# Optimization experiments

Hardware: AMD Instinct MI355X
Metric: run time of the kernel (lower is better)

Reference implementation:

```python
import jax, jax.numpy as jnp
import numpy as np

N = 50000          # nodes
E = 800000         # edges (avg degree 16)
D = 128            # feature dim
MSG_EPS = 1e-7     # GENConv eps added to relu(msg)
SM_EPS = 1e-16     # pyg softmax denominator eps
BN_EPS = 1e-5
LN_EPS = 1e-5


def setup_inputs() -> dict:
    key = jax.random.key(0)
    ks = jax.random.split(key, 6)
    x = jax.random.normal(ks[0], (N, D), dtype=jnp.float32)
    edge_index = jax.random.randint(ks[1], (2, E), 0, N, dtype=jnp.int32)
    t = jnp.array(1.0, dtype=jnp.float32)
    W1 = jax.random.normal(ks[2], (D, 2 * D), dtype=jnp.float32) / np.sqrt(D).astype(np.float32)
    b1 = jnp.zeros((2 * D,), jnp.float32)
    bn_gamma = jnp.ones((2 * D,), jnp.float32)
    bn_beta = jnp.zeros((2 * D,), jnp.float32)
    W2 = jax.random.normal(ks[3], (2 * D, D), dtype=jnp.float32) / np.sqrt(2 * D).astype(np.float32)
    b2 = jnp.zeros((D,), jnp.float32)
    ln_gamma = jnp.ones((D,), jnp.float32)
    ln_beta = jnp.zeros((D,), jnp.float32)
    return {"x": x, "edge_index": edge_index, "t": t, "W1": W1, "b1": b1,
            "bn_gamma": bn_gamma, "bn_beta": bn_beta, "W2": W2, "b2": b2,
            "ln_gamma": ln_gamma, "ln_beta": ln_beta}


def reference(x, edge_index, t, W1, b1, bn_gamma, bn_beta, W2, b2, ln_gamma, ln_beta):
    src, dst = edge_index[0], edge_index[1]
    # --- GENConv message: relu(x_j) + eps  -> [E, D]
    msg = jax.nn.relu(x[src]) + MSG_EPS
    # --- softmax aggregation over incoming edges per dst node, per feature
    logits = t * msg                                            # [E, D]
    seg_max = jax.ops.segment_max(logits, dst, num_segments=N)  # [N, D]
    seg_max = jnp.where(jnp.isfinite(seg_max), seg_max, 0.0)    # empty segments -> 0
    ex = jnp.exp(logits - seg_max[dst])                         # [E, D]
    denom = jax.ops.segment_sum(ex, dst, num_segments=N)        # [N, D]
    alpha = ex / (denom[dst] + SM_EPS)                          # [E, D]
    agg = jax.ops.segment_sum(alpha * msg, dst, num_segments=N) # [N, D]
    # --- GENConv update: MLP(agg + x), MLP = Lin(D,2D)->BN->ReLU->Lin(2D,D)
    h = agg + x
    h = h @ W1 + b1                                             # [N, 2D]
    mu = jnp.mean(h, axis=0)
    var = jnp.var(h, axis=0)
    h = (h - mu) * jax.lax.rsqrt(var + BN_EPS) * bn_gamma + bn_beta
    h = jax.nn.relu(h)
    h = h @ W2 + b2                                             # [N, D]
    # --- LayerNorm -> ReLU -> (dropout p=0 noop) -> residual
    mu2 = jnp.mean(h, axis=-1, keepdims=True)
    var2 = jnp.mean(jnp.square(h - mu2), axis=-1, keepdims=True)
    h = (h - mu2) * jax.lax.rsqrt(var2 + LN_EPS) * ln_gamma + ln_beta
    h = jax.nn.relu(h)
    return x + h
```

## Files before the change

### kernel.cpp

```cpp
#include <hip/hip_runtime.h>

#define D 128
#define D2 256
#define BSH 5
#define BNODES 32
#define NBMAX 2048
#define CAP 640
#define PCHUNK 4096

typedef __attribute__((ext_vector_type(8))) short short8;
typedef __attribute__((ext_vector_type(4))) float f32x4;

__device__ inline unsigned short f2b(float f) {
  unsigned u = __float_as_uint(f);
  unsigned r = (u + 0x7FFFu + ((u >> 16) & 1u)) >> 16;
  return (unsigned short)r;
}
__device__ inline float b2f(unsigned short h) {
  return __uint_as_float(((unsigned)h) << 16);
}
__device__ inline float lo2f(unsigned u) { return __uint_as_float(u << 16); }
__device__ inline float hi2f(unsigned u) { return __uint_as_float(u & 0xffff0000u); }

__global__ void convert_w_kernel(const float* __restrict__ W1,
                                 const float* __restrict__ W2,
                                 unsigned short* __restrict__ W1f,
                                 unsigned short* __restrict__ W2f) {
  int idx = blockIdx.x * 256 + threadIdx.x;
  if (idx < 32768) {
    int k = idx >> 8, n = idx & 255;
    int t = n >> 4, m16 = n & 15;
    int kk = k >> 5, quad = (k >> 3) & 3, j = k & 7;
    W1f[(((t * 4 + kk) * 64 + quad * 16 + m16) << 3) + j] = f2b(W1[idx]);
  } else {
    int i = idx - 32768;
    int k = i >> 7, n = i & 127;
    int t = n >> 4, m16 = n & 15;
    int kk = k >> 5, quad = (k >> 3) & 3, j = k & 7;
    W2f[(((t * 8 + kk) * 64 + quad * 16 + m16) << 3) + j] = f2b(W2[i]);
  }
}

__global__ void mb_kernel(const float* __restrict__ x, unsigned short* __restrict__ mb,
                          int total4) {
  int i = blockIdx.x * 256 + threadIdx.x;
  if (i < total4) {
    float4 v = reinterpret_cast<const float4*>(x)[i];
    unsigned lo = (unsigned)f2b(fmaxf(v.x, 0.f) + 1e-7f) |
                  ((unsigned)f2b(fmaxf(v.y, 0.f) + 1e-7f) << 16);
    unsigned hi = (unsigned)f2b(fmaxf(v.z, 0.f) + 1e-7f) |
                  ((unsigned)f2b(fmaxf(v.w, 0.f) + 1e-7f) << 16);
    reinterpret_cast<uint2*>(mb)[i] = make_uint2(lo, hi);
  } else if (i < total4 + 32) {
    reinterpret_cast<uint2*>(mb)[i] = make_uint2(0u, 0u);
  }
}

__global__ __launch_bounds__(256) void part_kernel(const int* __restrict__ ei,
                                                   int* __restrict__ cursor,
                                                   unsigned* __restrict__ pairbuf,
                                                   int E, int nb) {
  __shared__ int cnt[NBMAX];
  __shared__ int base[NBMAX];
  int tid = threadIdx.x;
  int c0 = blockIdx.x * PCHUNK;
  int nE = min(PCHUNK, E - c0);
  for (int i = tid; i < nb; i += 256) cnt[i] = 0;
  __syncthreads();
  for (int j = tid; j < nE; j += 256) {
    int dst = ei[E + c0 + j];
    atomicAdd(&cnt[dst >> BSH], 1);
  }
  __syncthreads();
  for (int i = tid; i < nb; i += 256) {
    int c = cnt[i];
    base[i] = (c > 0) ? atomicAdd(&cursor[i], c) : 0;
    cnt[i] = 0;
  }
  __syncthreads();
  for (int j = tid; j < nE; j += 256) {
    int e = c0 + j;
    int dst = ei[E + e];
    int src = ei[e];
    int b = dst >> BSH;
    int r = base[b] + atomicAdd(&cnt[b], 1);
    if (r < CAP)
      pairbuf[(size_t)b * CAP + r] =
          (unsigned)src | ((unsigned)(dst & (BNODES - 1)) << 16);
  }
}

__global__ __launch_bounds__(512) void agg2_kernel(const float* __restrict__ x,
                                                   const unsigned short* __restrict__ mb,
                                                   const unsigned* __restrict__ pairbuf,
                                                   const int* __restrict__ cursor,
                                                   const float* __restrict__ tptr,
                                                   unsigned short* __restrict__ h0b, int N) {
  __shared__ int soff[CAP + 4 * BNODES];
  __shared__ int cnt[BNODES], off[BNODES], run[BNODES], pcnt[BNODES];
  int b = blockIdx.x;
  int tid = threadIdx.x;
  int Eb = min(cursor[b], CAP);
  if (tid < BNODES) { cnt[tid] = 0; run[tid] = 0; }
  __syncthreads();
  for (int j = tid; j < Eb; j += 512)
    atomicAdd(&cnt[pairbuf[(size_t)b * CAP + j] >> 16], 1);
  __syncthreads();
  if (tid < BNODES) {
    int c = cnt[tid];
    int pc = (c + 3) & ~3;
    pcnt[tid] = pc;
    int s = pc;
#pragma unroll
    for (int st = 1; st < 32; st <<= 1) {
      int u = __shfl_up(s, st, 32);
      if ((tid & 31) >= st) s += u;
    }
    off[tid] = s - pc;
  }
  __syncthreads();
  for (int j = tid; j < Eb; j += 512) {
    unsigned p = pairbuf[(size_t)b * CAP + j];
    int dl = p >> 16;
    int r = atomicAdd(&run[dl], 1);
    soff[off[dl] + r] = (int)(p & 0xffffu) << 8;
  }
  if (tid < BNODES) {
    int o = off[tid];
    for (int r = cnt[tid]; r < pcnt[tid]; ++r) soff[o + r] = N << 8;
  }
  __syncthreads();

  int w = tid >> 6;
  int l = tid & 63;
  float t = tptr[0];
  int laneoff = l << 2;
  const char* mbase = (const char*)mb;
  for (int ln = w; ln < BNODES; ln += 8) {
    int n = (b << BSH) + ln;
    if (n >= N) continue;
    int s0 = off[ln];
    int dn = pcnt[ln];
    float den0 = 0.f, num0 = 0.f, den1 = 0.f, num1 = 0.f;
    if (dn > 0) {
      unsigned uu[4];
#pragma unroll
      for (int q = 0; q < 4; ++q)
        uu[q] = *(const unsigned*)(mbase + (soff[s0 + q] | laneoff));
      for (int j = 4; j < dn; j += 4) {
        unsigned vv[4];
#pragma unroll
        for (int q = 0; q < 4; ++q)
          vv[q] = *(const unsigned*)(mbase + (soff[s0 + j + q] | laneoff));
#pragma unroll
        for (int q = 0; q < 4; ++q) {
          float m0 = lo2f(uu[q]);
          float m1 = hi2f(uu[q]);
          float e0 = __expf(t * m0);
          float e1 = __expf(t * m1);
          den0 += e0; num0 += e0 * m0;
          den1 += e1; num1 += e1 * m1;
        }
#pragma unroll
        for (int q = 0; q < 4; ++q) uu[q] = vv[q];
      }
#pragma unroll
      for (int q = 0; q < 4; ++q) {
        float m0 = lo2f(uu[q]);
        float m1 = hi2f(uu[q]);
        float e0 = __expf(t * m0);
        float e1 = __expf(t * m1);
        den0 += e0; num0 += e0 * m0;
        den1 += e1; num1 += e1 * m1;
      }
      float fnpad = (float)(dn - cnt[ln]);
      den0 -= fnpad;
      den1 -= fnpad;
    }
    size_t idx = ((size_t)n << 7) + 2 * l;
    float2 xv = *reinterpret_cast<const float2*>(x + idx);
    float v0 = num0 / (den0 + 1e-16f) + xv.x;
    float v1 = num1 / (den1 + 1e-16f) + xv.y;
    *reinterpret_cast<unsigned*>(h0b + idx) =
        (unsigned)f2b(v0) | ((unsigned)f2b(v1) << 16);
  }
}

__global__ __launch_bounds__(256) void gemm1_mfma(
    const unsigned short* __restrict__ h0b, const unsigned short* __restrict__ W1f,
    unsigned short* __restrict__ h1b,
    float* __restrict__ bnsum, float* __restrict__ bnsumsq, int M) {
  __shared__ unsigned short lt[4][64][72];
  int tid = threadIdx.x;
  int w = tid >> 6;
  int l = tid & 63;
  int m16 = l & 15;
  int quad = l >> 4;
  int r0 = blockIdx.x * 64;

  f32x4 acc[4][4];
#pragma unroll
  for (int rt = 0; rt < 4; ++rt)
#pragma unroll
    for (int ct = 0; ct < 4; ++ct) acc[rt][ct] = (f32x4){0.f, 0.f, 0.f, 0.f};

#pragma unroll
  for (int kk = 0; kk < 4; ++kk) {
    short8 bfr[4];
#pragma unroll
    for (int ct = 0; ct < 4; ++ct)
      bfr[ct] = *reinterpret_cast<const short8*>(
          W1f + ((((w * 4 + ct) * 4 + kk) * 64 + l) << 3));
    short8 a[4];
#pragma unroll
    for (int rt = 0; rt < 4; ++rt) {
      int row = min(r0 + rt * 16 + m16, M - 1);
      a[rt] = *reinterpret_cast<const short8*>(h0b + (size_t)row * D + kk * 32 + quad * 8);
    }
#pragma unroll
    for (int rt = 0; rt < 4; ++rt)
#pragma unroll
      for (int ct = 0; ct < 4; ++ct)
        acc[rt][ct] = __builtin_amdgcn_mfma_f32_16x16x32_bf16(a[rt], bfr[ct], acc[rt][ct], 0, 0, 0);
  }

#pragma unroll
  for (int ct = 0; ct < 4; ++ct) {
    int col = w * 64 + ct * 16 + m16;
    float cs = 0.f, cq = 0.f;
#pragma unroll
    for (int rt = 0; rt < 4; ++rt) {
      int rloc = rt * 16 + quad * 4;
#pragma unroll
      for (int reg = 0; reg < 4; ++reg) {
        float val = acc[rt][ct][reg];
        if (r0 + rloc + reg < M) {
          cs += val;
          cq += val * val;
        }
        lt[w][rloc + reg][ct * 16 + m16] = f2b(val);
      }
    }
    cs += __shfl_xor(cs, 16, 64);
    cs += __shfl_xor(cs, 32, 64);
    cq += __shfl_xor(cq, 16, 64);
    cq += __shfl_xor(cq, 32, 64);
    if (quad == 0) {
      atomicAdd(&bnsum[col], cs);
      atomicAdd(&bnsumsq[col], cq);
    }
  }

  int row = r0 + l;
  if (row < M) {
    const unsigned short* src = &lt[w][l][0];
    unsigned short* dst = h1b + (size_t)row * D2 + w * 64;
#pragma unroll
    for (int j = 0; j < 8; ++j)
      *reinterpret_cast<short8*>(dst + j * 8) =
          *reinterpret_cast<const short8*>(src + j * 8);
  }
}

__global__ void bnfinal_kernel(const float* __restrict__ bnsum,
                               const float* __restrict__ bnsumsq,
                               const float* __restrict__ gamma,
                               const float* __restrict__ beta,
                               float* __restrict__ scale,
                               float* __restrict__ shift, int M) {
  int c = threadIdx.x;
  float invM = 1.f / (float)M;
  float mu = bnsum[c] * invM;
  float var = bnsumsq[c] * invM - mu * mu;
  float sc = gamma[c] * rsqrtf(var + 1e-5f);
  scale[c] = sc;
  shift[c] = beta[c] - mu * sc;
}

__global__ __launch_bounds__(256) void bnapply_kernel(
    unsigned short* __restrict__ h1b, const float* __restrict__ scale,
    const float* __restrict__ shift, int total8) {
  int i = blockIdx.x * 256 + threadIdx.x;
  if (i >= total8) return;
  int c0 = (i << 3) & 255;
  f32x4 sc0 = *reinterpret_cast<const f32x4*>(scale + c0);
  f32x4 sc1 = *reinterpret_cast<const f32x4*>(scale + c0 + 4);
  f32x4 sh0 = *reinterpret_cast<const f32x4*>(shift + c0);
  f32x4 sh1 = *reinterpret_cast<const f32x4*>(shift + c0 + 4);
  uint4 raw = reinterpret_cast<const uint4*>(h1b)[i];
  unsigned words[4] = {raw.x, raw.y, raw.z, raw.w};
  uint4 o;
  unsigned ow[4];
#pragma unroll
  for (int p = 0; p < 2; ++p) {
    f32x4 sc = p ? sc1 : sc0;
    f32x4 sh = p ? sh1 : sh0;
#pragma unroll
    for (int q = 0; q < 2; ++q) {
      unsigned u = words[p * 2 + q];
      float v0 = fmaxf(lo2f(u) * sc[q * 2] + sh[q * 2], 0.f);
      float v1 = fmaxf(hi2f(u) * sc[q * 2 + 1] + sh[q * 2 + 1], 0.f);
      ow[p * 2 + q] = (unsigned)f2b(v0) | ((unsigned)f2b(v1) << 16);
    }
  }
  o.x = ow[0]; o.y = ow[1]; o.z = ow[2]; o.w = ow[3];
  reinterpret_cast<uint4*>(h1b)[i] = o;
}

__global__ __launch_bounds__(256) void gemm2_mfma(
    const unsigned short* __restrict__ h1c, const unsigned short* __restrict__ W2f,
    const float* __restrict__ b2, const float* __restrict__ lng,
    const float* __restrict__ lnb, const float* __restrict__ x,
    float* __restrict__ out, int M) {
  __shared__ float lnp[64][2], lnp2[64][2];
  int tid = threadIdx.x;
  int w = tid >> 6;
  int l = tid & 63;
  int m16 = l & 15;
  int quad = l >> 4;
  int rb = w >> 1, cb = w & 1;
  int r00 = blockIdx.x * 64;

  f32x4 acc[2][4];
#pragma unroll
  for (int rt = 0; rt < 2; ++rt)
#pragma unroll
    for (int ct = 0; ct < 4; ++ct) acc[rt][ct] = (f32x4){0.f, 0.f, 0.f, 0.f};

#pragma unroll
  for (int kk = 0; kk < 8; ++kk) {
    short8 a[2];
#pragma unroll
    for (int rt = 0; rt < 2; ++rt) {
      int row = min(r00 + rb * 32 + rt * 16 + m16, M - 1);
      a[rt] = *reinterpret_cast<const short8*>(h1c + (size_t)row * D2 + kk * 32 + quad * 8);
    }
    short8 bfr[4];
#pragma unroll
    for (int ct = 0; ct < 4; ++ct)
      bfr[ct] = *reinterpret_cast<const short8*>(
          W2f + ((((cb * 4 + ct) * 8 + kk) * 64 + l) << 3));
#pragma unroll
    for (int rt = 0; rt < 2; ++rt)
#pragma unroll
      for (int ct = 0; ct < 4; ++ct)
        acc[rt][ct] = __builtin_amdgcn_mfma_f32_16x16x32_bf16(a[rt], bfr[ct], acc[rt][ct], 0, 0, 0);
  }

  float b2v[4], lgv[4], lbv[4];
#pragma unroll
  for (int ct = 0; ct < 4; ++ct) {
    int col = cb * 64 + ct * 16 + m16;
    b2v[ct] = b2[col];
    lgv[ct] = lng[col];
    lbv[ct] = lnb[col];
  }

#pragma unroll
  for (int rt = 0; rt < 2; ++rt) {
#pragma unroll
    for (int reg = 0; reg < 4; ++reg) {
      float s = 0.f, s2 = 0.f;
#pragma unroll
      for (int ct = 0; ct < 4; ++ct) {
        float v = acc[rt][ct][reg] + b2v[ct];
        s += v;
        s2 += v * v;
      }
#pragma unroll
      for (int msk = 1; msk < 16; msk <<= 1) {
        s += __shfl_xor(s, msk, 64);
        s2 += __shfl_xor(s2, msk, 64);
      }
      if (m16 == 0) {
        int rl = rb * 32 + rt * 16 + quad * 4 + reg;
        lnp[rl][cb] = s;
        lnp2[rl][cb] = s2;
      }
    }
  }
  __syncthreads();

#pragma unroll
  for (int rt = 0; rt < 2; ++rt) {
#pragma unroll
    for (int reg = 0; reg < 4; ++reg) {
      int rl = rb * 32 + rt * 16 + quad * 4 + reg;
      int row = r00 + rl;
      float s = lnp[rl][0] + lnp[rl][1];
      float s2 = lnp2[rl][0] + lnp2[rl][1];
      float mu = s * (1.f / 128.f);
      float var = s2 * (1.f / 128.f) - mu * mu;
      float inv = rsqrtf(var + 1e-5f);
      if (row < M) {
#pragma unroll
        for (int ct = 0; ct < 4; ++ct) {
          int col = cb * 64 + ct * 16 + m16;
          float v = acc[rt][ct][reg] + b2v[ct];
          float h = fmaxf((v - mu) * inv * lgv[ct] + lbv[ct], 0.f);
          out[(size_t)row * D + col] = x[(size_t)row * D + col] + h;
        }
      }
    }
  }
}

extern "C" void kernel_launch(void* const* d_in, const int* in_sizes, int n_in,
                              void* d_out, int out_size, void* d_ws, size_t ws_size,
                              hipStream_t stream) {
  const float* x   = (const float*)d_in[0];
  const int*   ei  = (const int*)d_in[1];
  const float* t   = (const float*)d_in[2];
  const float* W1  = (const float*)d_in[3];
  const float* bng = (const float*)d_in[5];
  const float* bnb = (const float*)d_in[6];
  const float* W2  = (const float*)d_in[7];
  const float* b2  = (const float*)d_in[8];
  const float* lng = (const float*)d_in[9];
  const float* lnb = (const float*)d_in[10];
  float* out = (float*)d_out;

  int N = in_sizes[0] / D;
  int E = in_sizes[1] / 2;
  size_t nd = (size_t)N * D;
  int nb = (N + BNODES - 1) >> BSH;

  unsigned short* mb  = (unsigned short*)d_ws;
  unsigned short* h0b = mb + nd + 128;
  unsigned short* h1b = h0b + nd;
  unsigned short* W1f = h1b + 2 * nd;
  unsigned short* W2f = W1f + 32768;
  float* bnsum   = (float*)(W2f + 32768);
  float* bnsumsq = bnsum + D2;
  float* bnscale = bnsumsq + D2;
  float* bnshift = bnscale + D2;
  int* cursor = (int*)(bnshift + D2);
  unsigned* pairbuf = (unsigned*)(cursor + NBMAX);

  hipMemsetAsync(bnsum, 0, (4 * D2 + NBMAX) * sizeof(int), stream);

  convert_w_kernel<<<256, 256, 0, stream>>>(W1, W2, W1f, W2f);
  int total4 = (int)(nd / 4);
  mb_kernel<<<(total4 + 32 + 255) / 256, 256, 0, stream>>>(x, mb, total4);

  part_kernel<<<(E + PCHUNK - 1) / PCHUNK, 256, 0, stream>>>(ei, cursor, pairbuf, E, nb);
  agg2_kernel<<<nb, 512, 0, stream>>>(x, mb, pairbuf, cursor, t, h0b, N);

  gemm1_mfma<<<(N + 63) / 64, 256, 0, stream>>>(h0b, W1f, h1b, bnsum, bnsumsq, N);
  bnfinal_kernel<<<1, 256, 0, stream>>>(bnsum, bnsumsq, bng, bnb, bnscale, bnshift, N);
  int total8 = (int)(2 * nd / 8);
  bnapply_kernel<<<(total8 + 255) / 256, 256, 0, stream>>>(h1b, bnscale, bnshift, total8);
  gemm2_mfma<<<(N + 63) / 64, 256, 0, stream>>>(h1b, W2f, b2, lng, lnb, x, out, N);
}
```

Before: 226.3 us.

## Fuse BN apply into gemm2 and spread BN-stat and cursor atomics

Removes the separate bnapply pass over the 2D-wide hidden buffer. BatchNorm scale/shift plus ReLU are now applied on the fly while loading the A operand in gemm2, with scale and shift staged in shared memory. BN sum and sum-of-squares atomics are spread across 32 replicas keyed by block index and reduced in bnfinal. Partition cursors are strided by 16 ints so they do not share cache lines. This saves one full read/write pass of h1 and a launch, and cuts atomic contention, at the cost of extra ALU work in gemm2's load path and a larger memset.

Result: faster. 211.3 us (-6.7%).

```diff
diff --git a/kernel.cpp b/kernel.cpp
--- a/kernel.cpp
+++ b/kernel.cpp
@@ -7,6 +7,8 @@
 #define NBMAX 2048
 #define CAP 640
 #define PCHUNK 4096
+#define REP 32
+#define CSTRIDE 16
 
 typedef __attribute__((ext_vector_type(8))) short short8;
 typedef __attribute__((ext_vector_type(4))) float f32x4;
@@ -74,7 +76,7 @@
   __syncthreads();
   for (int i = tid; i < nb; i += 256) {
     int c = cnt[i];
-    base[i] = (c > 0) ? atomicAdd(&cursor[i], c) : 0;
+    base[i] = (c > 0) ? atomicAdd(&cursor[i * CSTRIDE], c) : 0;
     cnt[i] = 0;
   }
   __syncthreads();
@@ -100,7 +102,7 @@
   __shared__ int cnt[BNODES], off[BNODES], run[BNODES], pcnt[BNODES];
   int b = blockIdx.x;
   int tid = threadIdx.x;
-  int Eb = min(cursor[b], CAP);
+  int Eb = min(cursor[b * CSTRIDE], CAP);
   if (tid < BNODES) { cnt[tid] = 0; run[tid] = 0; }
   __syncthreads();
   for (int j = tid; j < Eb; j += 512)
@@ -224,6 +226,7 @@
         acc[rt][ct] = __builtin_amdgcn_mfma_f32_16x16x32_bf16(a[rt], bfr[ct], acc[rt][ct], 0, 0, 0);
   }
 
+  int rep = (blockIdx.x & (REP - 1)) << 8;
 #pragma unroll
   for (int ct = 0; ct < 4; ++ct) {
     int col = w * 64 + ct * 16 + m16;
@@ -246,8 +249,8 @@
     cq += __shfl_xor(cq, 16, 64);
     cq += __shfl_xor(cq, 32, 64);
     if (quad == 0) {
-      atomicAdd(&bnsum[col], cs);
-      atomicAdd(&bnsumsq[col], cq);
+      atomicAdd(&bnsum[rep + col], cs);
+      atomicAdd(&bnsumsq[rep + col], cq);
     }
   }
 
@@ -269,51 +272,33 @@
                                float* __restrict__ scale,
                                float* __restrict__ shift, int M) {
   int c = threadIdx.x;
+  float s = 0.f, q = 0.f;
+#pragma unroll
+  for (int r = 0; r < REP; ++r) {
+    s += bnsum[(r << 8) + c];
+    q += bnsumsq[(r << 8) + c];
+  }
   float invM = 1.f / (float)M;
-  float mu = bnsum[c] * invM;
-  float var = bnsumsq[c] * invM - mu * mu;
+  float mu = s * invM;
+  float var = q * invM - mu * mu;
   float sc = gamma[c] * rsqrtf(var + 1e-5f);
   scale[c] = sc;
   shift[c] = beta[c] - mu * sc;
 }
 
-__global__ __launch_bounds__(256) void bnapply_kernel(
-    unsigned short* __restrict__ h1b, const float* __restrict__ scale,
-    const float* __restrict__ shift, int total8) {
-  int i = blockIdx.x * 256 + threadIdx.x;
-  if (i >= total8) return;
-  int c0 = (i << 3) & 255;
-  f32x4 sc0 = *reinterpret_cast<const f32x4*>(scale + c0);
-  f32x4 sc1 = *reinterpret_cast<const f32x4*>(scale + c0 + 4);
-  f32x4 sh0 = *reinterpret_cast<const f32x4*>(shift + c0);
-  f32x4 sh1 = *reinterpret_cast<const f32x4*>(shift + c0 + 4);
-  uint4 raw = reinterpret_cast<const uint4*>(h1b)[i];
-  unsigned words[4] = {raw.x, raw.y, raw.z, raw.w};
-  uint4 o;
-  unsigned ow[4];
-#pragma unroll
-  for (int p = 0; p < 2; ++p) {
-    f32x4 sc = p ? sc1 : sc0;
-    f32x4 sh = p ? sh1 : sh0;
-#pragma unroll
-    for (int q = 0; q < 2; ++q) {
-      unsigned u = words[p * 2 + q];
-      float v0 = fmaxf(lo2f(u) * sc[q * 2] + sh[q * 2], 0.f);
-      float v1 = fmaxf(hi2f(u) * sc[q * 2 + 1] + sh[q * 2 + 1], 0.f);
-      ow[p * 2 + q] = (unsigned)f2b(v0) | ((unsigned)f2b(v1) << 16);
-    }
-  }
-  o.x = ow[0]; o.y = ow[1]; o.z = ow[2]; o.w = ow[3];
-  reinterpret_cast<uint4*>(h1b)[i] = o;
-}
-
 __global__ __launch_bounds__(256) void gemm2_mfma(
-    const unsigned short* __restrict__ h1c, const unsigned short* __restrict__ W2f,
-    const float* __restrict__ b2, const float* __restrict__ lng,
+    const unsigned short* __restrict__ h1b, const unsigned short* __restrict__ W2f,
+    const float* __restrict__ b2, const float* __restrict__ bnscale,
+    const float* __restrict__ bnshift, const float* __restrict__ lng,
     const float* __restrict__ lnb, const float* __restrict__ x,
     float* __restrict__ out, int M) {
   __shared__ float lnp[64][2], lnp2[64][2];
+  __shared__ float sS[D2], sH[D2];
   int tid = threadIdx.x;
+  sS[tid] = bnscale[tid];
+  sH[tid] = bnshift[tid];
+  __syncthreads();
+
   int w = tid >> 6;
   int l = tid & 63;
   int m16 = l & 15;
@@ -329,11 +314,29 @@
 
 #pragma unroll
   for (int kk = 0; kk < 8; ++kk) {
+    int base = kk * 32 + quad * 8;
+    f32x4 s0 = *reinterpret_cast<const f32x4*>(&sS[base]);
+    f32x4 s1 = *reinterpret_cast<const f32x4*>(&sS[base + 4]);
+    f32x4 g0 = *reinterpret_cast<const f32x4*>(&sH[base]);
+    f32x4 g1 = *reinterpret_cast<const f32x4*>(&sH[base + 4]);
     short8 a[2];
 #pragma unroll
     for (int rt = 0; rt < 2; ++rt) {
       int row = min(r00 + rb * 32 + rt * 16 + m16, M - 1);
-      a[rt] = *reinterpret_cast<const short8*>(h1c + (size_t)row * D2 + kk * 32 + quad * 8);
+      uint4 raw = *reinterpret_cast<const uint4*>(h1b + (size_t)row * D2 + base);
+      unsigned wds[4] = {raw.x, raw.y, raw.z, raw.w};
+      unsigned ow[4];
+#pragma unroll
+      for (int q = 0; q < 4; ++q) {
+        f32x4 sv = (q < 2) ? s0 : s1;
+        f32x4 gv = (q < 2) ? g0 : g1;
+        int e = (q & 1) * 2;
+        float v0 = fmaxf(lo2f(wds[q]) * sv[e] + gv[e], 0.f);
+        float v1 = fmaxf(hi2f(wds[q]) * sv[e + 1] + gv[e + 1], 0.f);
+        ow[q] = (unsigned)f2b(v0) | ((unsigned)f2b(v1) << 16);
+      }
+      uint4 packed = make_uint4(ow[0], ow[1], ow[2], ow[3]);
+      a[rt] = *reinterpret_cast<short8*>(&packed);
     }
     short8 bfr[4];
 #pragma unroll
@@ -431,13 +434,13 @@
   unsigned short* W1f = h1b + 2 * nd;
   unsigned short* W2f = W1f + 32768;
   float* bnsum   = (float*)(W2f + 32768);
-  float* bnsumsq = bnsum + D2;
-  float* bnscale = bnsumsq + D2;
+  float* bnsumsq = bnsum + REP * 256;
+  int* cursor    = (int*)(bnsumsq + REP * 256);
+  float* bnscale = (float*)(cursor + NBMAX * CSTRIDE);
   float* bnshift = bnscale + D2;
-  int* cursor = (int*)(bnshift + D2);
-  unsigned* pairbuf = (unsigned*)(cursor + NBMAX);
-
-  hipMemsetAsync(bnsum, 0, (4 * D2 + NBMAX) * sizeof(int), stream);
+  unsigned* pairbuf = (unsigned*)(bnshift + D2);
+
+  hipMemsetAsync(bnsum, 0, (size_t)(2 * REP * 256 + NBMAX * CSTRIDE) * sizeof(int), stream);
 
   convert_w_kernel<<<256, 256, 0, stream>>>(W1, W2, W1f, W2f);
   int total4 = (int)(nd / 4);
@@ -448,7 +451,5 @@
 
   gemm1_mfma<<<(N + 63) / 64, 256, 0, stream>>>(h0b, W1f, h1b, bnsum, bnsumsq, N);
   bnfinal_kernel<<<1, 256, 0, stream>>>(bnsum, bnsumsq, bng, bnb, bnscale, bnshift, N);
-  int total8 = (int)(2 * nd / 8);
-  bnapply_kernel<<<(total8 + 255) / 256, 256, 0, stream>>>(h1b, bnscale, bnshift, total8);
-  gemm2_mfma<<<(N + 63) / 64, 256, 0, stream>>>(h1b, W2f, b2, lng, lnb, x, out, N);
-}
+  gemm2_mfma<<<(N + 63) / 64, 256, 0, stream>>>(h1b, W2f, b2, bnscale, bnshift, lng, lnb, x, out, N);
+}
```
